# Kernel optimization log

Hardware: AMD Instinct MI355X
Metric: run time of the kernel (lower is better)

Reference implementation:

```python
import jax, jax.numpy as jnp
import numpy as np

N_NODES = 50000
N_EDGES = 800000
IN_F = 96
HID = 64
N_CLS = 32


def setup_inputs() -> dict:
    key = jax.random.key(0)
    k1, k2, k3, k4 = jax.random.split(key, 4)
    x = jax.random.normal(k1, (N_NODES, IN_F), dtype=jnp.float32)
    edge_index = jax.random.randint(k2, (2, N_EDGES), 0, N_NODES, dtype=jnp.int64)
    # xavier_uniform init for weights, zeros for bias
    lim1 = float(np.sqrt(6.0 / (IN_F + HID)))
    lim2 = float(np.sqrt(6.0 / (HID + N_CLS)))
    W1 = jax.random.uniform(k3, (IN_F, HID), minval=-lim1, maxval=lim1, dtype=jnp.float32)
    W2 = jax.random.uniform(k4, (HID, N_CLS), minval=-lim2, maxval=lim2, dtype=jnp.float32)
    b1 = jnp.zeros((HID,), dtype=jnp.float32)
    b2 = jnp.zeros((N_CLS,), dtype=jnp.float32)
    return {"x": x, "edge_index": edge_index, "W1": W1, "b1": b1, "W2": W2, "b2": b2}


def _ghost_conv(h, src, dst, W, b, num_nodes):
    # gather neighbor feats per edge, per-edge matmul, scatter-add, bias
    msg = h[src] @ W                                   # [E, out]
    agg = jax.ops.segment_sum(msg, dst, num_segments=num_nodes)  # [N, out]
    return agg + b


def reference(x, edge_index, W1, b1, W2, b2):
    src, dst = edge_index[0], edge_index[1]
    n = x.shape[0]
    h = jax.nn.relu(_ghost_conv(x, src, dst, W1, b1, n))
    # F.dropout(training=False) is identity in eval mode
    out = _ghost_conv(h, src, dst, W2, b2, n)
    return jax.nn.log_softmax(out, axis=1)
```

## Files before the change

### kernel.cpp

```cpp
#include <hip/hip_runtime.h>
#include <hip/hip_bf16.h>

typedef __attribute__((ext_vector_type(8))) short bf16x8;
typedef __attribute__((ext_vector_type(4))) float f32x4;

#define NBLK 128
#define NBINS_PAD 800
#define BCAP 2048
#define W1LD 104

__device__ inline unsigned short f2bf(float f) {
    unsigned u = __float_as_uint(f);
    return (unsigned short)((u + 0x7fffu + ((u >> 16) & 1u)) >> 16);
}
__device__ inline unsigned pack2(float a, float b) {
    return (unsigned)f2bf(a) | ((unsigned)f2bf(b) << 16);
}
__device__ inline float blo(unsigned u) { return __uint_as_float(u << 16); }
__device__ inline float bhi(unsigned u) { return __uint_as_float(u & 0xffff0000u); }

__device__ inline void acc8(float* a, uint4 v) {
    a[0] += blo(v.x); a[1] += bhi(v.x);
    a[2] += blo(v.y); a[3] += bhi(v.y);
    a[4] += blo(v.z); a[5] += bhi(v.z);
    a[6] += blo(v.w); a[7] += bhi(v.w);
}

__global__ __launch_bounds__(256) void fused_hist_gemm1(
        const int* __restrict__ ei, int* __restrict__ counts, int E, int chunk, int nb,
        const float* __restrict__ W1, const float* __restrict__ W2,
        unsigned short* __restrict__ w2t,
        const float* __restrict__ X,
        unsigned short* __restrict__ y1a, unsigned short* __restrict__ y1b, int Mtiles) {
    __shared__ int hist[NBINS_PAD];
    __shared__ unsigned short w1l[64 * W1LD];
    int b = blockIdx.x, t = threadIdx.x;
    if (b < NBLK) {
        for (int i = t; i < NBINS_PAD; i += 256) hist[i] = 0;
        __syncthreads();
        int e0 = b * chunk;
        int n = E - e0; if (n > chunk) n = chunk; if (n < 0) n = 0;
        for (int i = t; i < n; i += 256) atomicAdd(&hist[ei[E + e0 + i] >> 6], 1);
        __syncthreads();
        for (int j = t; j < nb; j += 256) counts[j * NBLK + b] = hist[j];
        return;
    }
    if (b == NBLK) {
        for (int idx = t; idx < 64 * 32; idx += 256) {
            int n = idx / 64, k = idx - n * 64;
            w2t[idx] = f2bf(W2[k * 32 + n]);
        }
        return;
    }
    for (int idx = t; idx < 96 * 64; idx += 256) {
        int n = idx / 96, k = idx - n * 96;
        w1l[n * W1LD + k] = f2bf(W1[k * 64 + n]);
    }
    __syncthreads();
    int wave = (b - NBLK - 1) * 4 + (t >> 6);
    if (wave >= Mtiles) return;
    int lane = t & 63;
    int l15 = lane & 15, quad = lane >> 4;
    const float* arow = X + (long)(wave * 16 + l15) * 96 + quad * 8;
    f32x4 acc[4] = {{0,0,0,0},{0,0,0,0},{0,0,0,0},{0,0,0,0}};
#pragma unroll
    for (int tt = 0; tt < 3; ++tt) {
        float4 p0 = *(const float4*)(arow + tt * 32);
        float4 p1 = *(const float4*)(arow + tt * 32 + 4);
        union { bf16x8 v; unsigned u[4]; } a;
        a.u[0] = pack2(p0.x, p0.y); a.u[1] = pack2(p0.z, p0.w);
        a.u[2] = pack2(p1.x, p1.y); a.u[3] = pack2(p1.z, p1.w);
#pragma unroll
        for (int nt = 0; nt < 4; ++nt) {
            bf16x8 bfr = *(const bf16x8*)(w1l + (nt * 16 + l15) * W1LD + tt * 32 + quad * 8);
            acc[nt] = __builtin_amdgcn_mfma_f32_16x16x32_bf16(a.v, bfr, acc[nt], 0, 0, 0);
        }
    }
    int mbase = wave * 16 + quad * 4;
#pragma unroll
    for (int nt = 0; nt < 4; ++nt) {
        int col = nt * 16 + l15;
        unsigned short* slab = (col < 32) ? y1a : y1b;
        int colh = col & 31;
#pragma unroll
        for (int r = 0; r < 4; ++r)
            slab[(long)(mbase + r) * 32 + colh] = f2bf(acc[nt][r]);
    }
}

__global__ __launch_bounds__(256) void rowscan(int* __restrict__ counts,
                                               int* __restrict__ btot, int nb) {
    int w = (blockIdx.x * 256 + threadIdx.x) >> 6;
    int lane = threadIdx.x & 63;
    if (w >= nb) return;
    int* row = counts + (size_t)w * NBLK;
    int c0 = row[lane * 2], c1 = row[lane * 2 + 1];
    int s = c0 + c1;
#pragma unroll
    for (int o = 1; o < 64; o <<= 1) {
        int tt = __shfl_up(s, o);
        if (lane >= o) s += tt;
    }
    int excl = s - (c0 + c1);
    row[lane * 2] = excl;
    row[lane * 2 + 1] = excl + c0;
    if (lane == 63) btot[w] = s;
}

__global__ __launch_bounds__(256) void blk_place(const int* __restrict__ ei,
                                                 const int* __restrict__ counts,
                                                 unsigned* __restrict__ pairs,
                                                 int E, int chunk, int nb) {
    __shared__ int cur[NBINS_PAD];
    int b = blockIdx.x, t = threadIdx.x;
    for (int j = t; j < nb; j += 256) cur[j] = (j << 11) + counts[j * NBLK + b];
    __syncthreads();
    int e0 = b * chunk;
    int n = E - e0; if (n > chunk) n = chunk; if (n < 0) n = 0;
    for (int i = t; i < n; i += 256) {
        int s = ei[e0 + i], d = ei[E + e0 + i];
        int j = d >> 6;
        int pos = atomicAdd(&cur[j], 1);
        if (pos < ((j + 1) << 11))
            pairs[pos] = (unsigned)s | ((unsigned)(d & 63) << 16);
    }
}

__global__ __launch_bounds__(256) void bucket_build(const unsigned* __restrict__ pairs,
                                                    const int* __restrict__ btot,
                                                    int2* __restrict__ noderange,
                                                    int* __restrict__ srcs, int N) {
    __shared__ unsigned spk[BCAP];
    __shared__ int stage[BCAP];
    __shared__ int cnt64[64], cur64[64];
    int b = blockIdx.x, t = threadIdx.x;
    int base = b << 11;
    int cnt = btot[b]; if (cnt > BCAP) cnt = BCAP;
    if (t < 64) cnt64[t] = 0;
    __syncthreads();
    for (int i = t; i < cnt; i += 256) {
        unsigned p = pairs[base + i];
        spk[i] = p;
        atomicAdd(&cnt64[(p >> 16) & 63], 1);
    }
    __syncthreads();
    if (t < 64) {
        int v = cnt64[t], x = v;
#pragma unroll
        for (int o = 1; o < 64; o <<= 1) {
            int y = __shfl_up(x, o);
            if (t >= o) x += y;
        }
        int excl = x - v;
        cur64[t] = excl;
        int node = b * 64 + t;
        if (node < N) noderange[node] = make_int2(base + excl, base + excl + v);
    }
    __syncthreads();
    for (int i = t; i < cnt; i += 256) {
        unsigned p = spk[i];
        int pos = atomicAdd(&cur64[(p >> 16) & 63], 1);
        stage[pos] = (int)(p & 0xffffu);
    }
    __syncthreads();
    for (int i = t; i < cnt; i += 256) srcs[base + i] = stage[i];
}

__global__ void gather_relu_half(const uint4* __restrict__ y1h, const int2* __restrict__ rng,
                                 const int* __restrict__ srcs, const float* __restrict__ biash,
                                 uint4* __restrict__ hh, int N) {
    int gid = blockIdx.x * blockDim.x + threadIdx.x;
    int n = gid >> 1;
    if (n >= N) return;
    int q = gid & 1;
    int2 r01 = rng[n];
    int s0 = r01.x, s1 = r01.y;
    float a[16];
#pragma unroll
    for (int i = 0; i < 16; ++i) a[i] = 0.f;
    const uint4* base = y1h + q * 2;
    int e = s0;
    for (; e + 4 <= s1; e += 4) {
        long r0 = (long)srcs[e] * 4, r1 = (long)srcs[e + 1] * 4;
        long r2 = (long)srcs[e + 2] * 4, r3 = (long)srcs[e + 3] * 4;
        uint4 u0a = base[r0], u0b = base[r0 + 1];
        uint4 u1a = base[r1], u1b = base[r1 + 1];
        uint4 u2a = base[r2], u2b = base[r2 + 1];
        uint4 u3a = base[r3], u3b = base[r3 + 1];
        acc8(a, u0a); acc8(a + 8, u0b);
        acc8(a, u1a); acc8(a + 8, u1b);
        acc8(a, u2a); acc8(a + 8, u2b);
        acc8(a, u3a); acc8(a + 8, u3b);
    }
    for (; e < s1; ++e) {
        long r = (long)srcs[e] * 4;
        uint4 ua = base[r], ub = base[r + 1];
        acc8(a, ua); acc8(a + 8, ub);
    }
    const float* bq = biash + q * 16;
#pragma unroll
    for (int i = 0; i < 16; ++i) a[i] = fmaxf(a[i] + bq[i], 0.f);
    uint4 o0, o1;
    o0.x = pack2(a[0], a[1]);   o0.y = pack2(a[2], a[3]);
    o0.z = pack2(a[4], a[5]);   o0.w = pack2(a[6], a[7]);
    o1.x = pack2(a[8], a[9]);   o1.y = pack2(a[10], a[11]);
    o1.z = pack2(a[12], a[13]); o1.w = pack2(a[14], a[15]);
    hh[(long)n * 4 + q * 2] = o0;
    hh[(long)n * 4 + q * 2 + 1] = o1;
}

__global__ void mfma_gemm2(const unsigned short* __restrict__ hA,
                           const unsigned short* __restrict__ hB,
                           const unsigned short* __restrict__ Bt,
                           unsigned short* __restrict__ Y, int Mtiles) {
    int wave = blockIdx.x * 4 + (threadIdx.x >> 6);
    if (wave >= Mtiles) return;
    int lane = threadIdx.x & 63;
    int l15 = lane & 15, quad = lane >> 4;
    long arow = (long)(wave * 16 + l15) * 32 + quad * 8;
    f32x4 acc[2] = {{0,0,0,0},{0,0,0,0}};
#pragma unroll
    for (int t = 0; t < 2; ++t) {
        const unsigned short* hs = t ? hB : hA;
        bf16x8 af = *(const bf16x8*)(hs + arow);
#pragma unroll
        for (int nt = 0; nt < 2; ++nt) {
            bf16x8 bfr = *(const bf16x8*)(Bt + (long)(nt * 16 + l15) * 64 + t * 32 + quad * 8);
            acc[nt] = __builtin_amdgcn_mfma_f32_16x16x32_bf16(af, bfr, acc[nt], 0, 0, 0);
        }
    }
    int mbase = wave * 16 + quad * 4;
#pragma unroll
    for (int nt = 0; nt < 2; ++nt) {
        int col = nt * 16 + l15;
#pragma unroll
        for (int r = 0; r < 4; ++r)
            Y[(long)(mbase + r) * 32 + col] = f2bf(acc[nt][r]);
    }
}

__global__ void gather_lsm(const uint4* __restrict__ y2, const int2* __restrict__ rng,
                           const int* __restrict__ srcs, const float* __restrict__ bias,
                           float* __restrict__ out, int N) {
    int gid = blockIdx.x * blockDim.x + threadIdx.x;
    int n = gid >> 1;
    if (n >= N) return;
    int half = gid & 1;
    int2 r01 = rng[n];
    int s0 = r01.x, s1 = r01.y;
    float a[16];
#pragma unroll
    for (int i = 0; i < 16; ++i) a[i] = 0.f;
    const uint4* base = y2 + half * 2;
    int e = s0;
    for (; e + 4 <= s1; e += 4) {
        long r0 = (long)srcs[e] * 4, r1 = (long)srcs[e + 1] * 4;
        long r2 = (long)srcs[e + 2] * 4, r3 = (long)srcs[e + 3] * 4;
        uint4 u0a = base[r0], u0b = base[r0 + 1];
        uint4 u1a = base[r1], u1b = base[r1 + 1];
        uint4 u2a = base[r2], u2b = base[r2 + 1];
        uint4 u3a = base[r3], u3b = base[r3 + 1];
        acc8(a, u0a); acc8(a + 8, u0b);
        acc8(a, u1a); acc8(a + 8, u1b);
        acc8(a, u2a); acc8(a + 8, u2b);
        acc8(a, u3a); acc8(a + 8, u3b);
    }
    for (; e < s1; ++e) {
        long r = (long)srcs[e] * 4;
        uint4 ua = base[r], ub = base[r + 1];
        acc8(a, ua); acc8(a + 8, ub);
    }
    const float* bq = bias + half * 16;
    float m = -1e30f;
#pragma unroll
    for (int i = 0; i < 16; ++i) { a[i] += bq[i]; m = fmaxf(m, a[i]); }
    m = fmaxf(m, __shfl_xor(m, 1));
    float s = 0.f;
#pragma unroll
    for (int i = 0; i < 16; ++i) s += __expf(a[i] - m);
    s += __shfl_xor(s, 1);
    float ls = m + __logf(s);
    float* op = out + (long)n * 32 + half * 16;
#pragma unroll
    for (int i = 0; i < 16; ++i) op[i] = a[i] - ls;
}

extern "C" void kernel_launch(void* const* d_in, const int* in_sizes, int n_in,
                              void* d_out, int out_size, void* d_ws, size_t ws_size,
                              hipStream_t stream) {
    const float* x  = (const float*)d_in[0];
    const int*   ei = (const int*)d_in[1];
    const float* W1 = (const float*)d_in[2];
    const float* b1 = (const float*)d_in[3];
    const float* W2 = (const float*)d_in[4];
    const float* b2 = (const float*)d_in[5];
    float* out = (float*)d_out;

    const int N = in_sizes[0] / 96;
    const int E = in_sizes[1] / 2;
    const int nb = (N + 63) / 64;
    const int chunk = (E + NBLK - 1) / NBLK;

    char* p = (char*)d_ws;
    unsigned short* y1a = (unsigned short*)p;     p += (size_t)N * 32 * 2;
    unsigned short* y1b = (unsigned short*)p;     p += (size_t)N * 32 * 2;
    unsigned short* hA  = (unsigned short*)p;     p += (size_t)N * 32 * 2;
    unsigned short* hB  = (unsigned short*)p;     p += (size_t)N * 32 * 2;
    unsigned short* y2  = (unsigned short*)p;     p += (size_t)N * 32 * 2;
    unsigned short* w2t = (unsigned short*)p;     p += 64 * 32 * 2;
    int2* noderange = (int2*)p;                   p += (size_t)N * 8;
    int* counts = (int*)p;                        p += ((size_t)nb * NBLK * 4 + 12) & ~15ull;
    int* btot   = (int*)p;                        p += ((size_t)nb * 4 + 12) & ~15ull;
    unsigned* pairs = (unsigned*)p;               p += (size_t)nb * BCAP * 4;
    int* srcs   = (int*)p;                        p += (size_t)nb * BCAP * 4;

    const int Mtiles = N / 16;
    const int gblocks = (Mtiles + 3) / 4;

    fused_hist_gemm1<<<NBLK + 1 + gblocks, 256, 0, stream>>>(
        ei, counts, E, chunk, nb, W1, W2, w2t, x, y1a, y1b, Mtiles);
    rowscan<<<(nb * 64 + 255) / 256, 256, 0, stream>>>(counts, btot, nb);
    blk_place<<<NBLK, 256, 0, stream>>>(ei, counts, pairs, E, chunk, nb);
    bucket_build<<<nb, 256, 0, stream>>>(pairs, btot, noderange, srcs, N);

    {
        int grid = (N * 2 + 255) / 256;
        gather_relu_half<<<grid, 256, 0, stream>>>(
            (const uint4*)y1a, noderange, srcs, b1, (uint4*)hA, N);
        gather_relu_half<<<grid, 256, 0, stream>>>(
            (const uint4*)y1b, noderange, srcs, b1 + 32, (uint4*)hB, N);
    }

    mfma_gemm2<<<gblocks, 256, 0, stream>>>(hA, hB, w2t, y2, Mtiles);

    gather_lsm<<<(N * 2 + 255) / 256, 256, 0, stream>>>(
        (const uint4*)y2, noderange, srcs, b2, out, N);
}
```

Baseline: 162.2 us.

## Fuse bucket build, layer-1 gather+ReLU, and GEMM2 into one kernel

Merges the per-bucket CSR build, the two half-width layer-1 gather/bias/ReLU passes and the second MFMA GEMM into a single kernel with one block per 64-node bucket. Source indices stay in shared memory for the gather, and the hidden tile is staged in LDS (padded stride) and fed straight to MFMA. This removes three launches and the global round trip of the hidden activations. In exchange, occupancy drops: only 782 blocks run, LDS use per block grows, and 4 threads per node gather at 16-byte width.

```diff
diff --git a/kernel.cpp b/kernel.cpp
--- a/kernel.cpp
+++ b/kernel.cpp
@@ -8,6 +8,7 @@
 #define NBINS_PAD 800
 #define BCAP 2048
 #define W1LD 104
+#define HLD 72
 
 __device__ inline unsigned short f2bf(float f) {
     unsigned u = __float_as_uint(f);
@@ -126,13 +127,16 @@
     }
 }
 
-__global__ __launch_bounds__(256) void bucket_build(const unsigned* __restrict__ pairs,
-                                                    const int* __restrict__ btot,
-                                                    int2* __restrict__ noderange,
-                                                    int* __restrict__ srcs, int N) {
+__global__ __launch_bounds__(256) void bucket_fused(
+        const unsigned* __restrict__ pairs, const int* __restrict__ btot,
+        const uint4* __restrict__ y1a, const uint4* __restrict__ y1b,
+        const float* __restrict__ b1, const unsigned short* __restrict__ w2t,
+        int2* __restrict__ noderange, int* __restrict__ srcs,
+        unsigned short* __restrict__ y2, int N) {
     __shared__ unsigned spk[BCAP];
-    __shared__ int stage[BCAP];
-    __shared__ int cnt64[64], cur64[64];
+    __shared__ int lsrc[BCAP];
+    __shared__ int cnt64[64], cur64[64], rs[64], re[64];
+    __shared__ unsigned short htile[64 * HLD];
     int b = blockIdx.x, t = threadIdx.x;
     int base = b << 11;
     int cnt = btot[b]; if (cnt > BCAP) cnt = BCAP;
@@ -153,6 +157,8 @@
         }
         int excl = x - v;
         cur64[t] = excl;
+        rs[t] = excl;
+        re[t] = excl + v;
         int node = b * 64 + t;
         if (node < N) noderange[node] = make_int2(base + excl, base + excl + v);
     }
@@ -160,82 +166,70 @@
     for (int i = t; i < cnt; i += 256) {
         unsigned p = spk[i];
         int pos = atomicAdd(&cur64[(p >> 16) & 63], 1);
-        stage[pos] = (int)(p & 0xffffu);
-    }
-    __syncthreads();
-    for (int i = t; i < cnt; i += 256) srcs[base + i] = stage[i];
-}
-
-__global__ void gather_relu_half(const uint4* __restrict__ y1h, const int2* __restrict__ rng,
-                                 const int* __restrict__ srcs, const float* __restrict__ biash,
-                                 uint4* __restrict__ hh, int N) {
-    int gid = blockIdx.x * blockDim.x + threadIdx.x;
-    int n = gid >> 1;
-    if (n >= N) return;
-    int q = gid & 1;
-    int2 r01 = rng[n];
-    int s0 = r01.x, s1 = r01.y;
+        lsrc[pos] = (int)(p & 0xffffu);
+    }
+    __syncthreads();
+    for (int i = t; i < cnt; i += 256) srcs[base + i] = lsrc[i];
+
+    int dl = t >> 2, q = t & 3;
+    int s0 = rs[dl], s1 = re[dl];
     float a[16];
 #pragma unroll
     for (int i = 0; i < 16; ++i) a[i] = 0.f;
-    const uint4* base = y1h + q * 2;
-    int e = s0;
-    for (; e + 4 <= s1; e += 4) {
-        long r0 = (long)srcs[e] * 4, r1 = (long)srcs[e + 1] * 4;
-        long r2 = (long)srcs[e + 2] * 4, r3 = (long)srcs[e + 3] * 4;
-        uint4 u0a = base[r0], u0b = base[r0 + 1];
-        uint4 u1a = base[r1], u1b = base[r1 + 1];
-        uint4 u2a = base[r2], u2b = base[r2 + 1];
-        uint4 u3a = base[r3], u3b = base[r3 + 1];
-        acc8(a, u0a); acc8(a + 8, u0b);
-        acc8(a, u1a); acc8(a + 8, u1b);
-        acc8(a, u2a); acc8(a + 8, u2b);
-        acc8(a, u3a); acc8(a + 8, u3b);
-    }
-    for (; e < s1; ++e) {
-        long r = (long)srcs[e] * 4;
-        uint4 ua = base[r], ub = base[r + 1];
-        acc8(a, ua); acc8(a + 8, ub);
-    }
-    const float* bq = biash + q * 16;
-#pragma unroll
-    for (int i = 0; i < 16; ++i) a[i] = fmaxf(a[i] + bq[i], 0.f);
-    uint4 o0, o1;
-    o0.x = pack2(a[0], a[1]);   o0.y = pack2(a[2], a[3]);
-    o0.z = pack2(a[4], a[5]);   o0.w = pack2(a[6], a[7]);
-    o1.x = pack2(a[8], a[9]);   o1.y = pack2(a[10], a[11]);
-    o1.z = pack2(a[12], a[13]); o1.w = pack2(a[14], a[15]);
-    hh[(long)n * 4 + q * 2] = o0;
-    hh[(long)n * 4 + q * 2 + 1] = o1;
-}
-
-__global__ void mfma_gemm2(const unsigned short* __restrict__ hA,
-                           const unsigned short* __restrict__ hB,
-                           const unsigned short* __restrict__ Bt,
-                           unsigned short* __restrict__ Y, int Mtiles) {
-    int wave = blockIdx.x * 4 + (threadIdx.x >> 6);
-    if (wave >= Mtiles) return;
-    int lane = threadIdx.x & 63;
+#pragma unroll
+    for (int half = 0; half < 2; ++half) {
+        const uint4* ybase = (half ? y1b : y1a) + q;
+        float* ah = a + half * 8;
+        int e = s0;
+        for (; e + 8 <= s1; e += 8) {
+            uint4 u0 = ybase[(long)lsrc[e] * 4],     u1 = ybase[(long)lsrc[e + 1] * 4];
+            uint4 u2 = ybase[(long)lsrc[e + 2] * 4], u3 = ybase[(long)lsrc[e + 3] * 4];
+            uint4 u4 = ybase[(long)lsrc[e + 4] * 4], u5 = ybase[(long)lsrc[e + 5] * 4];
+            uint4 u6 = ybase[(long)lsrc[e + 6] * 4], u7 = ybase[(long)lsrc[e + 7] * 4];
+            acc8(ah, u0); acc8(ah, u1); acc8(ah, u2); acc8(ah, u3);
+            acc8(ah, u4); acc8(ah, u5); acc8(ah, u6); acc8(ah, u7);
+        }
+        for (; e < s1; ++e) acc8(ah, ybase[(long)lsrc[e] * 4]);
+    }
+    {
+        const float* bqA = b1 + q * 8;
+        const float* bqB = b1 + 32 + q * 8;
+        float v[16];
+#pragma unroll
+        for (int j = 0; j < 8; ++j) v[j] = fmaxf(a[j] + bqA[j], 0.f);
+#pragma unroll
+        for (int j = 0; j < 8; ++j) v[8 + j] = fmaxf(a[8 + j] + bqB[j], 0.f);
+        uint4 o0, o1;
+        o0.x = pack2(v[0], v[1]);   o0.y = pack2(v[2], v[3]);
+        o0.z = pack2(v[4], v[5]);   o0.w = pack2(v[6], v[7]);
+        o1.x = pack2(v[8], v[9]);   o1.y = pack2(v[10], v[11]);
+        o1.z = pack2(v[12], v[13]); o1.w = pack2(v[14], v[15]);
+        *(uint4*)(htile + dl * HLD + q * 8) = o0;
+        *(uint4*)(htile + dl * HLD + 32 + q * 8) = o1;
+    }
+    __syncthreads();
+    int w = t >> 6, lane = t & 63;
     int l15 = lane & 15, quad = lane >> 4;
-    long arow = (long)(wave * 16 + l15) * 32 + quad * 8;
-    f32x4 acc[2] = {{0,0,0,0},{0,0,0,0}};
-#pragma unroll
-    for (int t = 0; t < 2; ++t) {
-        const unsigned short* hs = t ? hB : hA;
-        bf16x8 af = *(const bf16x8*)(hs + arow);
+    const unsigned short* arow = htile + (w * 16 + l15) * HLD + quad * 8;
+    f32x4 acc2[2] = {{0,0,0,0},{0,0,0,0}};
+#pragma unroll
+    for (int t2 = 0; t2 < 2; ++t2) {
+        bf16x8 af = *(const bf16x8*)(arow + t2 * 32);
 #pragma unroll
         for (int nt = 0; nt < 2; ++nt) {
-            bf16x8 bfr = *(const bf16x8*)(Bt + (long)(nt * 16 + l15) * 64 + t * 32 + quad * 8);
-            acc[nt] = __builtin_amdgcn_mfma_f32_16x16x32_bf16(af, bfr, acc[nt], 0, 0, 0);
-        }
-    }
-    int mbase = wave * 16 + quad * 4;
+            bf16x8 bfr = *(const bf16x8*)(w2t + (long)(nt * 16 + l15) * 64 + t2 * 32 + quad * 8);
+            acc2[nt] = __builtin_amdgcn_mfma_f32_16x16x32_bf16(af, bfr, acc2[nt], 0, 0, 0);
+        }
+    }
+    int mbase = b * 64 + w * 16 + quad * 4;
 #pragma unroll
     for (int nt = 0; nt < 2; ++nt) {
         int col = nt * 16 + l15;
 #pragma unroll
-        for (int r = 0; r < 4; ++r)
-            Y[(long)(mbase + r) * 32 + col] = f2bf(acc[nt][r]);
+        for (int r = 0; r < 4; ++r) {
+            int n = mbase + r;
+            if (n < N) y2[(long)n * 32 + col] = f2bf(acc2[nt][r]);
+        }
     }
 }
 
@@ -304,8 +298,6 @@
     char* p = (char*)d_ws;
     unsigned short* y1a = (unsigned short*)p;     p += (size_t)N * 32 * 2;
     unsigned short* y1b = (unsigned short*)p;     p += (size_t)N * 32 * 2;
-    unsigned short* hA  = (unsigned short*)p;     p += (size_t)N * 32 * 2;
-    unsigned short* hB  = (unsigned short*)p;     p += (size_t)N * 32 * 2;
     unsigned short* y2  = (unsigned short*)p;     p += (size_t)N * 32 * 2;
     unsigned short* w2t = (unsigned short*)p;     p += 64 * 32 * 2;
     int2* noderange = (int2*)p;                   p += (size_t)N * 8;
@@ -321,18 +313,8 @@
         ei, counts, E, chunk, nb, W1, W2, w2t, x, y1a, y1b, Mtiles);
     rowscan<<<(nb * 64 + 255) / 256, 256, 0, stream>>>(counts, btot, nb);
     blk_place<<<NBLK, 256, 0, stream>>>(ei, counts, pairs, E, chunk, nb);
-    bucket_build<<<nb, 256, 0, stream>>>(pairs, btot, noderange, srcs, N);
-
-    {
-        int grid = (N * 2 + 255) / 256;
-        gather_relu_half<<<grid, 256, 0, stream>>>(
-            (const uint4*)y1a, noderange, srcs, b1, (uint4*)hA, N);
-        gather_relu_half<<<grid, 256, 0, stream>>>(
-            (const uint4*)y1b, noderange, srcs, b1 + 32, (uint4*)hB, N);
-    }
-
-    mfma_gemm2<<<gblocks, 256, 0, stream>>>(hA, hB, w2t, y2, Mtiles);
-
+    bucket_fused<<<nb, 256, 0, stream>>>(pairs, btot, (const uint4*)y1a, (const uint4*)y1b,
+                                         b1, w2t, noderange, srcs, y2, N);
     gather_lsm<<<(N * 2 + 255) / 256, 256, 0, stream>>>(
         (const uint4*)y2, noderange, srcs, b2, out, N);
 }
```

New measurement: 146.9 us. 9.4% less time.
